# Kernel tuning notes

Hardware: AMD Instinct MI355X
Metric: run time of the kernel (lower is better)

The kernel has to match this reference:

```python
import jax, jax.numpy as jnp
import numpy as np

NQ = 12          # qubits per node circuit
DIM = 2 ** NQ    # statevector length 4096


def _apply_1q(state, U, w):
    """Apply 2x2 gate U (shared (2,2) or per-batch (B,2,2)) on wire w. state: (B, 4096)."""
    B = state.shape[0]
    l, r = 2 ** w, 2 ** (NQ - w - 1)
    s = state.reshape(B, l, 2, r)
    if U.ndim == 2:
        s = jnp.einsum('ij,bajc->baic', U, s)
    else:
        s = jnp.einsum('bij,bajc->baic', U, s)
    return s.reshape(B, DIM)


_G = np.zeros((2, 2, 2, 2), np.complex64)  # CNOT tensor: (c_out, t_out, c_in, t_in)
for _c in range(2):
    for _t in range(2):
        _G[_c, _t ^ _c, _c, _t] = 1.0


def _apply_cnot(state, c, t):
    B = state.shape[0]
    lo, hi = min(c, t), max(c, t)
    a, m, r = 2 ** lo, 2 ** (hi - lo - 1), 2 ** (NQ - hi - 1)
    s = state.reshape(B, a, 2, m, 2, r)
    T = _G if c == lo else _G.transpose(1, 0, 3, 2)  # reorder to (lo, hi) axis convention
    s = jnp.einsum('ijkl,bakcld->baicjd', jnp.asarray(T), s)
    return s.reshape(B, DIM)


def _ry_mats(ang):
    """Per-node RY matrices. ang: (B,) -> (B,2,2) complex64."""
    c, s = jnp.cos(ang / 2), jnp.sin(ang / 2)
    U = jnp.stack([jnp.stack([c, -s], -1), jnp.stack([s, c], -1)], -2)
    return U.astype(jnp.complex64)


def _rot_mat(p):
    """PennyLane Rot(phi, theta, omega) = RZ(omega) RY(theta) RZ(phi)."""
    phi, th, om = p[0], p[1], p[2]
    c, s = jnp.cos(th / 2), jnp.sin(th / 2)
    U = jnp.stack([
        jnp.stack([jnp.exp(-0.5j * (phi + om)) * c, -jnp.exp(0.5j * (phi - om)) * s]),
        jnp.stack([jnp.exp(-0.5j * (phi - om)) * s, jnp.exp(0.5j * (phi + om)) * c]),
    ])
    return U.astype(jnp.complex64)


# (rot_wire_a, rot_wire_b, (cnot_control, cnot_target)) blocks of the TTN circuit
_BLOCKS = [(0, 1, (0, 1)), (2, 3, (3, 2)), (4, 5, (4, 5)), (6, 7, (7, 6)),
           (8, 9, (8, 9)), (10, 11, (11, 10)), (1, 2, (1, 2)), (5, 6, (6, 5)),
           (9, 10, (10, 9)), (2, 5, (2, 5)), (5, 9, (5, 9))]


def _ttn_circuit(M, theta):
    """Batched 12-qubit TTN circuit. M: (B,12) angles, theta: (69,). Returns <Z_9>: (B,)."""
    B = M.shape[0]
    state = jnp.zeros((B, DIM), jnp.complex64).at[:, 0].set(1.0)
    for w in range(NQ):
        state = _apply_1q(state, _ry_mats(M[:, w]), w)
    k = 0
    for w1, w2, (c, t) in _BLOCKS:
        state = _apply_1q(state, _rot_mat(theta[3 * k:3 * k + 3]), w1); k += 1
        state = _apply_1q(state, _rot_mat(theta[3 * k:3 * k + 3]), w2); k += 1
        state = _apply_cnot(state, c, t)
    state = _apply_1q(state, _rot_mat(theta[3 * k:3 * k + 3]), 4)  # final Rot, k = 22
    probs = (state.real ** 2 + state.imag ** 2).reshape(B, 2 ** 9, 2, 2 ** 2)
    return probs[:, :, 0].sum((1, 2)) - probs[:, :, 1].sum((1, 2))  # <Z on wire 9>


def setup_inputs() -> dict:
    key = jax.random.key(0)
    kx, ke, ki, ko, kt = jax.random.split(key, 5)
    N, E, D = 1024, 8192, 4
    X = jax.random.normal(kx, (N, D), dtype=jnp.float32)
    e = jax.random.uniform(ke, (E,), dtype=jnp.float32)
    idx_i = jax.random.randint(ki, (E,), 0, N)
    idx_o = jax.random.randint(ko, (E,), 0, N)
    Ri = jnp.zeros((N, E), jnp.float32).at[idx_i, jnp.arange(E)].set(1.0)
    Ro = jnp.zeros((N, E), jnp.float32).at[idx_o, jnp.arange(E)].set(1.0)
    theta = jax.random.uniform(kt, (69,), dtype=jnp.float32, maxval=2 * np.pi)
    return {"X": X, "e": e, "Ri": Ri, "Ro": Ro, "theta": theta}


def reference(X, e, Ri, Ro, theta):
    bo = Ro.T @ X                     # [E, D] features of outgoing nodes
    bi = Ri.T @ X                     # [E, D]
    mi = (Ri * e) @ bo                # [N, D] edge-weighted aggregation
    mo = (Ro * e) @ bi                # [N, D]
    M = jnp.concatenate([mi, mo, X], axis=1)   # [N, 12] -> circuit angles
    z = _ttn_circuit(M, theta)
    return (jnp.pi * (1.0 - z)).astype(jnp.float32)  # 2*pi*(1 - <Z>)/2 per node
```

## Files before the change

kernel.cpp:

```cpp
#include <hip/hip_runtime.h>
#include <math.h>

#define NN 1024
#define NE 8192

struct c32 { float x, y; };
__device__ __forceinline__ c32 cmul(c32 a, c32 b)  { return {a.x*b.x - a.y*b.y, a.x*b.y + a.y*b.x}; }
__device__ __forceinline__ c32 cmulc(c32 a, c32 b) { return {a.x*b.x + a.y*b.y, a.y*b.x - a.x*b.y}; }
__device__ __forceinline__ c32 cadd(c32 a, c32 b)  { return {a.x + b.x, a.y + b.y}; }

__device__ __forceinline__ float sx(float v, int m)  { return __shfl_xor(v, m, 64); }
__device__ __forceinline__ float sidx(float v, int l){ return __shfl(v, l, 64); }

__device__ __forceinline__ void rot2(const float* __restrict__ t3, c32 A[2][2]) {
  float phi = t3[0], th = t3[1], om = t3[2];
  float s, c;   __sincosf(0.5f * th, &s, &c);
  float sa, ca; __sincosf(0.5f * (phi + om), &sa, &ca);
  float sb, cb; __sincosf(0.5f * (phi - om), &sb, &cb);
  A[0][0] = {  ca * c, -sa * c };
  A[0][1] = { -cb * s, -sb * s };
  A[1][0] = {  cb * s, -sb * s };
  A[1][1] = {  ca * c,  sa * c };
}

__device__ __forceinline__ void rot_lane(c32* a, const c32 (*U)[2], int lane, int b) {
  int s = (lane >> b) & 1;
  c32 us = s ? U[1][1] : U[0][0];
  c32 up = s ? U[1][0] : U[0][1];
  #pragma unroll
  for (int r = 0; r < 4; r++) {
    c32 p = { sx(a[r].x, 1 << b), sx(a[r].y, 1 << b) };
    a[r] = cadd(cmul(us, a[r]), cmul(up, p));
  }
}
__device__ __forceinline__ void rot_pair(c32& x0, c32& x1, const c32 (*U)[2]) {
  c32 n0 = cadd(cmul(U[0][0], x0), cmul(U[0][1], x1));
  c32 n1 = cadd(cmul(U[1][0], x0), cmul(U[1][1], x1));
  x0 = n0; x1 = n1;
}
__device__ __forceinline__ void cnot_ll(c32* a, int lane, int c, int t) {
  int idx = lane ^ (((lane >> c) & 1) << t);
  #pragma unroll
  for (int r = 0; r < 4; r++) a[r] = { sidx(a[r].x, idx), sidx(a[r].y, idx) };
}
__device__ __forceinline__ void rotB(c32* bb, const c32 (*U)[2], int k) {
  int mask = (1 << k) - 1;
  #pragma unroll
  for (int t = 0; t < 8; t++) {
    int i0 = ((t & ~mask) << 1) | (t & mask);
    int i1 = i0 | (1 << k);
    c32 b0 = bb[i0], b1 = bb[i1];
    bb[i0] = cadd(cmul(U[0][0], b0), cmul(U[0][1], b1));
    bb[i1] = cadd(cmul(U[1][0], b0), cmul(U[1][1], b1));
  }
}
__device__ __forceinline__ void cnotB(c32* bb, int c, int t) {
  int lo = c < t ? c : t, hi = c < t ? t : c;
  int lm = (1 << lo) - 1, hm = (1 << hi) - 1;
  #pragma unroll
  for (int q = 0; q < 4; q++) {
    int x = ((q & ~lm) << 1) | (q & lm);
    x = ((x & ~hm) << 1) | (x & hm);
    int i0 = x | (1 << c), i1 = i0 | (1 << t);
    c32 tmp = bb[i0]; bb[i0] = bb[i1]; bb[i1] = tmp;
  }
}

__global__ void __launch_bounds__(256) k_extract(const float* __restrict__ Ri,
                                                 const float* __restrict__ Ro,
                                                 int* __restrict__ idx_i,
                                                 int* __restrict__ idx_o,
                                                 float* __restrict__ mimo) {
  int q = blockIdx.x * 256 + threadIdx.x;
  if (q < 2048) ((float4*)mimo)[q] = make_float4(0.f, 0.f, 0.f, 0.f);
  float4 a = ((const float4*)Ri)[q];
  float4 b = ((const float4*)Ro)[q];
  int n = q >> 11;
  int k = (q << 2) & (NE - 1);
  if (a.x != 0.f) idx_i[k + 0] = n;
  if (a.y != 0.f) idx_i[k + 1] = n;
  if (a.z != 0.f) idx_i[k + 2] = n;
  if (a.w != 0.f) idx_i[k + 3] = n;
  if (b.x != 0.f) idx_o[k + 0] = n;
  if (b.y != 0.f) idx_o[k + 1] = n;
  if (b.z != 0.f) idx_o[k + 2] = n;
  if (b.w != 0.f) idx_o[k + 3] = n;
}

__global__ void k_edges(const float* __restrict__ X, const float* __restrict__ e,
                        const int* __restrict__ idx_i, const int* __restrict__ idx_o,
                        float* __restrict__ mimo) {
  int k = blockIdx.x * blockDim.x + threadIdx.x;
  if (k >= NE) return;
  int ni = idx_i[k], no = idx_o[k];
  float w = e[k];
  float4 xo = ((const float4*)X)[no];
  float4 xi = ((const float4*)X)[ni];
  atomicAdd(&mimo[ni * 4 + 0], w * xo.x);
  atomicAdd(&mimo[ni * 4 + 1], w * xo.y);
  atomicAdd(&mimo[ni * 4 + 2], w * xo.z);
  atomicAdd(&mimo[ni * 4 + 3], w * xo.w);
  atomicAdd(&mimo[4096 + no * 4 + 0], w * xi.x);
  atomicAdd(&mimo[4096 + no * 4 + 1], w * xi.y);
  atomicAdd(&mimo[4096 + no * 4 + 2], w * xi.z);
  atomicAdd(&mimo[4096 + no * 4 + 3], w * xi.w);
}

__global__ void __launch_bounds__(256) k_circuit(const float* __restrict__ X,
                                                 const float* __restrict__ theta,
                                                 const float* __restrict__ mimo,
                                                 float* __restrict__ out) {
  __shared__ c32 R[23][2][2];
  const int tid = threadIdx.x;
  if (tid < 23) {
    c32 A[2][2];
    rot2(theta + 3 * tid, A);
    R[tid][0][0] = A[0][0]; R[tid][0][1] = A[0][1];
    R[tid][1][0] = A[1][0]; R[tid][1][1] = A[1][1];
  }
  __syncthreads();

  const int lane = tid & 63;
  const int n = (blockIdx.x << 2) | (tid >> 6);

  float4 miv = ((const float4*)mimo)[n];
  float4 mov = ((const float4*)mimo)[1024 + n];
  float4 xv  = ((const float4*)X)[n];
  float ang[12] = { miv.x, miv.y, miv.z, miv.w, mov.x, mov.y, mov.z, mov.w, xv.x, xv.y, xv.z, xv.w };
  float cw[12], sw[12];
  #pragma unroll
  for (int w = 0; w < 12; w++) __sincosf(0.5f * ang[w], &sw[w], &cw[w]);

  float q00 = 0.f, q11 = 0.f; c32 q01 = {0.f, 0.f};
  {
    c32 bb[16];
    #pragma unroll
    for (int i = 0; i < 16; i++) {
      float amp = 1.f;
      #pragma unroll
      for (int w = 8; w < 12; w++) amp *= ((i >> (11 - w)) & 1) ? sw[w] : cw[w];
      bb[i] = { amp, 0.f };
    }
    rotB(bb, R[8], 3);  rotB(bb, R[9], 2);  cnotB(bb, 3, 2);
    rotB(bb, R[10], 1); rotB(bb, R[11], 0); cnotB(bb, 0, 1);
    rotB(bb, R[16], 2); rotB(bb, R[17], 1); cnotB(bb, 1, 2);
    #pragma unroll
    for (int ao = 0; ao < 8; ao++) {
      int i0 = ((ao & ~3) << 1) | (ao & 3);
      int i1 = i0 | 4;
      c32 b0 = bb[i0], b1 = bb[i1];
      q00 += b0.x * b0.x + b0.y * b0.y;
      q11 += b1.x * b1.x + b1.y * b1.y;
      q01 = cadd(q01, cmulc(b0, b1));
    }
  }

  c32 a[4];
  {
    float lfac = 1.f;
    #pragma unroll
    for (int w = 2; w < 8; w++) lfac *= ((lane >> (7 - w)) & 1) ? sw[w] : cw[w];
    a[0] = { cw[0] * cw[1] * lfac, 0.f };
    a[1] = { cw[0] * sw[1] * lfac, 0.f };
    a[2] = { sw[0] * cw[1] * lfac, 0.f };
    a[3] = { sw[0] * sw[1] * lfac, 0.f };
  }
  rot_pair(a[0], a[2], R[0]);  rot_pair(a[1], a[3], R[0]);
  rot_pair(a[0], a[1], R[1]);  rot_pair(a[2], a[3], R[1]);
  { c32 t = a[2]; a[2] = a[3]; a[3] = t; }
  rot_lane(a, R[2], lane, 5);
  rot_lane(a, R[3], lane, 4);
  cnot_ll(a, lane, 4, 5);
  rot_lane(a, R[4], lane, 3);
  rot_lane(a, R[5], lane, 2);
  cnot_ll(a, lane, 3, 2);
  rot_lane(a, R[6], lane, 1);
  rot_lane(a, R[7], lane, 0);
  cnot_ll(a, lane, 0, 1);
  rot_pair(a[0], a[1], R[12]); rot_pair(a[2], a[3], R[12]);
  rot_lane(a, R[13], lane, 5);
  a[1] = { sx(a[1].x, 32), sx(a[1].y, 32) };
  a[3] = { sx(a[3].x, 32), sx(a[3].y, 32) };
  rot_lane(a, R[14], lane, 2);
  rot_lane(a, R[15], lane, 1);
  cnot_ll(a, lane, 1, 2);
  rot_lane(a, R[18], lane, 5);
  rot_lane(a, R[19], lane, 2);
  cnot_ll(a, lane, 5, 2);
  rot_lane(a, R[22], lane, 3);

  int s5 = (lane >> 2) & 1;
  float p00 = 0.f, p11 = 0.f; c32 p01 = {0.f, 0.f};
  #pragma unroll
  for (int r = 0; r < 4; r++) {
    c32 pr = { sx(a[r].x, 4), sx(a[r].y, 4) };
    float nn = a[r].x * a[r].x + a[r].y * a[r].y;
    c32 cp = cmulc(a[r], pr);
    p00 += s5 ? 0.f : nn;
    p11 += s5 ? nn : 0.f;
    p01.x += s5 ? 0.f : cp.x;
    p01.y += s5 ? 0.f : cp.y;
  }
  #pragma unroll
  for (int m = 1; m < 64; m <<= 1) {
    p00 += sx(p00, m); p11 += sx(p11, m);
    p01.x += sx(p01.x, m); p01.y += sx(p01.y, m);
  }

  c32 U4[4][4];
  #pragma unroll
  for (int i = 0; i < 2; i++)
    #pragma unroll
    for (int p = 0; p < 2; p++)
      #pragma unroll
      for (int j = 0; j < 2; j++)
        #pragma unroll
        for (int q = 0; q < 2; q++)
          U4[2 * i + p][2 * j + q] = cmul(R[20][i][j], R[21][p][q]);
  #pragma unroll
  for (int c = 0; c < 4; c++) { c32 t = U4[2][c]; U4[2][c] = U4[3][c]; U4[3][c] = t; }

  c32 rho5[2][2] = { {{p00, 0.f}, p01}, {{p01.x, -p01.y}, {p11, 0.f}} };
  c32 rho9[2][2] = { {{q00, 0.f}, q01}, {{q01.x, -q01.y}, {q11, 0.f}} };
  float z = 0.f;
  #pragma unroll
  for (int aa = 0; aa < 4; aa++)
    #pragma unroll
    for (int b2 = 0; b2 < 4; b2++) {
      c32 m = {0.f, 0.f};
      #pragma unroll
      for (int i = 0; i < 4; i++) {
        c32 t = cmulc(U4[i][aa], U4[i][b2]);
        if (i & 1) { m.x -= t.x; m.y -= t.y; } else { m = cadd(m, t); }
      }
      c32 rr = cmul(rho5[aa >> 1][b2 >> 1], rho9[aa & 1][b2 & 1]);
      z += m.x * rr.x - m.y * rr.y;
    }

  if (lane == 0) out[n] = 3.14159265358979f * (1.f - z);
}

extern "C" void kernel_launch(void* const* d_in, const int* in_sizes, int n_in,
                              void* d_out, int out_size, void* d_ws, size_t ws_size,
                              hipStream_t stream) {
  (void)in_sizes; (void)n_in; (void)out_size; (void)ws_size;
  const float* X     = (const float*)d_in[0];
  const float* e     = (const float*)d_in[1];
  const float* Ri    = (const float*)d_in[2];
  const float* Ro    = (const float*)d_in[3];
  const float* theta = (const float*)d_in[4];
  float* out = (float*)d_out;

  char* ws = (char*)d_ws;
  int*   idx_i = (int*)(ws);
  int*   idx_o = (int*)(ws + 32768);
  float* mimo  = (float*)(ws + 65536);

  const int per4 = NN * NE / 4;
  hipLaunchKernelGGL(k_extract, dim3(per4 / 256), dim3(256), 0, stream, Ri, Ro, idx_i, idx_o, mimo);
  hipLaunchKernelGGL(k_edges,   dim3(NE / 256), dim3(256), 0, stream, X, e, idx_i, idx_o, mimo);
  hipLaunchKernelGGL(k_circuit, dim3(NN / 4), dim3(256), 0, stream, X, theta, mimo, out);
}
```

Before: 40.24 us.

## Fuse edge aggregation and circuit kernels via cooperative launch with grid barrier

```diff
diff --git a/kernel.cpp b/kernel.cpp
--- a/kernel.cpp
+++ b/kernel.cpp
@@ -70,9 +70,11 @@
                                                  const float* __restrict__ Ro,
                                                  int* __restrict__ idx_i,
                                                  int* __restrict__ idx_o,
-                                                 float* __restrict__ mimo) {
+                                                 float* __restrict__ mimo,
+                                                 int* __restrict__ cnt) {
   int q = blockIdx.x * 256 + threadIdx.x;
   if (q < 2048) ((float4*)mimo)[q] = make_float4(0.f, 0.f, 0.f, 0.f);
+  if (q == 0) *cnt = 0;
   float4 a = ((const float4*)Ri)[q];
   float4 b = ((const float4*)Ro)[q];
   int n = q >> 11;
@@ -87,46 +89,62 @@
   if (b.w != 0.f) idx_o[k + 3] = n;
 }
 
-__global__ void k_edges(const float* __restrict__ X, const float* __restrict__ e,
-                        const int* __restrict__ idx_i, const int* __restrict__ idx_o,
-                        float* __restrict__ mimo) {
-  int k = blockIdx.x * blockDim.x + threadIdx.x;
-  if (k >= NE) return;
-  int ni = idx_i[k], no = idx_o[k];
-  float w = e[k];
-  float4 xo = ((const float4*)X)[no];
-  float4 xi = ((const float4*)X)[ni];
-  atomicAdd(&mimo[ni * 4 + 0], w * xo.x);
-  atomicAdd(&mimo[ni * 4 + 1], w * xo.y);
-  atomicAdd(&mimo[ni * 4 + 2], w * xo.z);
-  atomicAdd(&mimo[ni * 4 + 3], w * xo.w);
-  atomicAdd(&mimo[4096 + no * 4 + 0], w * xi.x);
-  atomicAdd(&mimo[4096 + no * 4 + 1], w * xi.y);
-  atomicAdd(&mimo[4096 + no * 4 + 2], w * xi.z);
-  atomicAdd(&mimo[4096 + no * 4 + 3], w * xi.w);
-}
-
-__global__ void __launch_bounds__(256) k_circuit(const float* __restrict__ X,
-                                                 const float* __restrict__ theta,
-                                                 const float* __restrict__ mimo,
-                                                 float* __restrict__ out) {
+__global__ void __launch_bounds__(256) k_ec2(const float* __restrict__ X,
+                                             const float* __restrict__ e,
+                                             const float* __restrict__ theta,
+                                             const int* __restrict__ idx_i,
+                                             const int* __restrict__ idx_o,
+                                             float* __restrict__ mimo,
+                                             int* __restrict__ cnt,
+                                             float* __restrict__ out) {
   __shared__ c32 R[23][2][2];
-  const int tid = threadIdx.x;
+  const int tid  = threadIdx.x;
+  const int gtid = blockIdx.x * 256 + tid;
+
   if (tid < 23) {
     c32 A[2][2];
     rot2(theta + 3 * tid, A);
     R[tid][0][0] = A[0][0]; R[tid][0][1] = A[0][1];
     R[tid][1][0] = A[1][0]; R[tid][1][1] = A[1][1];
   }
+
+  if (gtid < NE) {
+    int ni = idx_i[gtid], no = idx_o[gtid];
+    float w = e[gtid];
+    float4 xo = ((const float4*)X)[no];
+    float4 xi = ((const float4*)X)[ni];
+    atomicAdd(&mimo[ni * 4 + 0], w * xo.x);
+    atomicAdd(&mimo[ni * 4 + 1], w * xo.y);
+    atomicAdd(&mimo[ni * 4 + 2], w * xo.z);
+    atomicAdd(&mimo[ni * 4 + 3], w * xo.w);
+    atomicAdd(&mimo[4096 + no * 4 + 0], w * xi.x);
+    atomicAdd(&mimo[4096 + no * 4 + 1], w * xi.y);
+    atomicAdd(&mimo[4096 + no * 4 + 2], w * xi.z);
+    atomicAdd(&mimo[4096 + no * 4 + 3], w * xi.w);
+  }
+
   __syncthreads();
+  __threadfence();
+  if (tid == 0) {
+    atomicAdd(cnt, 1);
+    while (__hip_atomic_load(cnt, __ATOMIC_RELAXED, __HIP_MEMORY_SCOPE_AGENT) < 256) {}
+  }
+  __syncthreads();
+  __threadfence();
 
   const int lane = tid & 63;
   const int n = (blockIdx.x << 2) | (tid >> 6);
 
-  float4 miv = ((const float4*)mimo)[n];
-  float4 mov = ((const float4*)mimo)[1024 + n];
-  float4 xv  = ((const float4*)X)[n];
-  float ang[12] = { miv.x, miv.y, miv.z, miv.w, mov.x, mov.y, mov.z, mov.w, xv.x, xv.y, xv.z, xv.w };
+  float av = 0.f;
+  if (lane < 8) {
+    int off = (lane < 4) ? (n * 4 + lane) : (4096 + n * 4 + (lane - 4));
+    av = atomicAdd(&mimo[off], 0.0f);
+  }
+  float ang[12];
+  #pragma unroll
+  for (int i = 0; i < 8; i++) ang[i] = sidx(av, i);
+  float4 xv = ((const float4*)X)[n];
+  ang[8] = xv.x; ang[9] = xv.y; ang[10] = xv.z; ang[11] = xv.w;
   float cw[12], sw[12];
   #pragma unroll
   for (int w = 0; w < 12; w++) __sincosf(0.5f * ang[w], &sw[w], &cw[w]);
@@ -255,9 +273,13 @@
   int*   idx_i = (int*)(ws);
   int*   idx_o = (int*)(ws + 32768);
   float* mimo  = (float*)(ws + 65536);
+  int*   cnt   = (int*)(ws + 98304);
 
   const int per4 = NN * NE / 4;
-  hipLaunchKernelGGL(k_extract, dim3(per4 / 256), dim3(256), 0, stream, Ri, Ro, idx_i, idx_o, mimo);
-  hipLaunchKernelGGL(k_edges,   dim3(NE / 256), dim3(256), 0, stream, X, e, idx_i, idx_o, mimo);
-  hipLaunchKernelGGL(k_circuit, dim3(NN / 4), dim3(256), 0, stream, X, theta, mimo, out);
-}
+  hipLaunchKernelGGL(k_extract, dim3(per4 / 256), dim3(256), 0, stream,
+                     Ri, Ro, idx_i, idx_o, mimo, cnt);
+
+  void* args[] = { (void*)&X, (void*)&e, (void*)&theta, (void*)&idx_i, (void*)&idx_o,
+                   (void*)&mimo, (void*)&cnt, (void*)&out };
+  hipLaunchCooperativeKernel((const void*)k_ec2, dim3(256), dim3(256), args, 0, stream);
+}
```

Result: slower. 92.09 us (+128.8%).
